# Performance work log

Measured on AMD Instinct MI355X. Metric: run time of the kernel, lower is better.

Reference implementation:

```python
import jax, jax.numpy as jnp
import numpy as np

N = 50000
E = 1600000
IN_DIM = 128
H = 8
D = 16  # out_dim per head


def setup_inputs() -> dict:
    key = jax.random.key(0)
    ks = jax.random.split(key, 9)
    h = jax.random.normal(ks[0], (N, IN_DIM), dtype=jnp.float32)
    src = jax.random.randint(ks[1], (E,), 0, N, dtype=jnp.int32)
    dst = jax.random.randint(ks[2], (E,), 0, N, dtype=jnp.int32)
    s = 1.0 / np.sqrt(IN_DIM)
    WQ = jax.random.uniform(ks[3], (IN_DIM, H * D), jnp.float32, -s, s)
    WK = jax.random.uniform(ks[4], (IN_DIM, H * D), jnp.float32, -s, s)
    WV = jax.random.uniform(ks[5], (IN_DIM, H * D), jnp.float32, -s, s)
    bQ = jax.random.uniform(ks[6], (H * D,), jnp.float32, -s, s)
    bK = jax.random.uniform(ks[7], (H * D,), jnp.float32, -s, s)
    bV = jax.random.uniform(ks[8], (H * D,), jnp.float32, -s, s)
    return {"h": h, "src": src, "dst": dst, "WQ": WQ, "WK": WK, "WV": WV,
            "bQ": bQ, "bK": bK, "bV": bV}


def reference(h, src, dst, WQ, WK, WV, bQ, bK, bV):
    # Node projections -> [N, H, D]
    Q = (h @ WQ + bQ).reshape(-1, H, D)
    K = (h @ WK + bK).reshape(-1, H, D)
    V = (h @ WV + bV).reshape(-1, H, D)
    # Edge scores: dot(K[src], Q[dst]) per head, scaled+clamped exp -> [E, H]
    scale = jnp.float32(np.sqrt(D))
    score = jnp.exp(jnp.clip(jnp.sum(K[src] * Q[dst], axis=-1) / scale, -5.0, 5.0))
    # Scatter-sum to destination nodes
    wV = jax.ops.segment_sum(score[:, :, None] * V[src], dst, num_segments=N)  # [N, H, D]
    z = jax.ops.segment_sum(score, dst, num_segments=N)  # [N, H]
    return wV / z[:, :, None]
```

## Files before the change

kernel.cpp:

```cpp
#include <hip/hip_runtime.h>

#define N_NODES 50000
#define N_PAD   50048
#define N_EDGES 1600000
#define HD 128
#define CHUNK 4096
#define NCHUNK ((N_EDGES + CHUNK - 1) / CHUNK)
#define NBUCKET ((N_NODES + 127) / 128)
#define PROJ_BLOCKS (N_PAD / 64)

typedef __attribute__((ext_vector_type(8))) short short8;
typedef __attribute__((ext_vector_type(4))) float floatx4;
typedef __attribute__((ext_vector_type(2))) float float2v;

union U4S8 { uint4 u; short8 s; };

__device__ __forceinline__ unsigned short f2bf(float f) {
    unsigned u = __float_as_uint(f);
    unsigned r = (u + 0x7fffu + ((u >> 16) & 1u)) >> 16;
    return (unsigned short)r;
}

__global__ __launch_bounds__(256) void k_chunkhist(
    const int* __restrict__ dst, int* __restrict__ chunkhist, int* __restrict__ btot,
    const float* __restrict__ WQ, const float* __restrict__ WK, const float* __restrict__ WV,
    unsigned short* __restrict__ Wf) {
    int t = threadIdx.x, c = blockIdx.x;
    if (c >= NCHUNK) {
        int tid = (c - NCHUNK) * 256 + t;
        int lane = tid & 63;
        int kstep = (tid >> 6) & 3;
        int ntile = tid >> 8;
        int g = ntile >> 3;
        int col = (ntile & 7) * 16 + (lane & 15);
        int k0 = kstep * 32 + (lane >> 4) * 8;
        const float* W = (g == 0) ? WQ : (g == 1) ? WK : WV;
        unsigned short r[8];
#pragma unroll
        for (int j = 0; j < 8; ++j)
            r[j] = f2bf(W[(size_t)(k0 + j) * HD + col]);
        *(uint4*)(Wf + (size_t)tid * 8) = *(uint4*)r;
        return;
    }
    __shared__ int hist[NBUCKET];
    for (int i = t; i < NBUCKET; i += 256) hist[i] = 0;
    __syncthreads();
    int e0 = c * CHUNK;
    int cnt = min(CHUNK, N_EDGES - e0);
    const uint4* d4 = (const uint4*)(dst + e0);
    int cnt4 = cnt >> 2;
    for (int i = t; i < cnt4; i += 256) {
        uint4 v = d4[i];
        atomicAdd(&hist[v.x >> 7], 1);
        atomicAdd(&hist[v.y >> 7], 1);
        atomicAdd(&hist[v.z >> 7], 1);
        atomicAdd(&hist[v.w >> 7], 1);
    }
    __syncthreads();
    for (int i = t; i < NBUCKET; i += 256) {
        int v = hist[i];
        chunkhist[c * NBUCKET + i] = v;
        if (v) atomicAdd(&btot[i], v);
    }
}

__global__ __launch_bounds__(256) void k_choff(const int* __restrict__ chunkhist,
                                               const int* __restrict__ btot,
                                               int* __restrict__ bucket_ptr,
                                               int* __restrict__ chunkoff) {
    int b = blockIdx.x, t = threadIdx.x;
    int x = 0;
    for (int i = t; i < NBUCKET; i += 256)
        if (i < b) x += btot[i];
    __shared__ int red[256];
    red[t] = x;
    __syncthreads();
    for (int off = 128; off > 0; off >>= 1) {
        if (t < off) red[t] += red[t + off];
        __syncthreads();
    }
    int base = red[0];
    if (t == 0) {
        bucket_ptr[b] = base;
        if (b == NBUCKET - 1) bucket_ptr[NBUCKET] = base + btot[b];
    }
    const int PER = (NCHUNK + 255) / 256;
    int c0 = t * PER;
    int v[PER];
    int s = 0;
#pragma unroll
    for (int i = 0; i < PER; ++i) {
        int c = c0 + i;
        v[i] = (c < NCHUNK) ? chunkhist[c * NBUCKET + b] : 0;
        s += v[i];
    }
    __shared__ int part[256];
    part[t] = s;
    __syncthreads();
    for (int off = 1; off < 256; off <<= 1) {
        int y = (t >= off) ? part[t - off] : 0;
        __syncthreads();
        part[t] += y;
        __syncthreads();
    }
    int run = base + part[t] - s;
#pragma unroll
    for (int i = 0; i < PER; ++i) {
        int c = c0 + i;
        if (c < NCHUNK) { chunkoff[c * NBUCKET + b] = run; run += v[i]; }
    }
}

__global__ __launch_bounds__(256) void k_scatter_proj(
    const int* __restrict__ src, const int* __restrict__ dst,
    const int* __restrict__ chunkoff, int* __restrict__ packed,
    const float* __restrict__ h, const unsigned short* __restrict__ Wf,
    const float* __restrict__ bQ, const float* __restrict__ bK, const float* __restrict__ bV,
    float* __restrict__ Qo, unsigned short* __restrict__ Kb, unsigned short* __restrict__ Vb) {
    int c = blockIdx.x;
    int t = threadIdx.x;
    if (c >= NCHUNK) {
        int blk = c - NCHUNK;
        int w = t >> 6;
        int l = t & 63;
        int row0 = blk * 64 + w * 16;
        int arow = row0 + (l & 15);
        int akoff = (l >> 4) * 8;
        bool rowok = arow < N_NODES;

        short8 a[4];
#pragma unroll
        for (int ks = 0; ks < 4; ++ks) {
            unsigned short r[8];
            if (rowok) {
                const float4* ap = (const float4*)(h + (size_t)arow * HD + ks * 32 + akoff);
                float4 f0 = ap[0], f1 = ap[1];
                r[0] = f2bf(f0.x); r[1] = f2bf(f0.y); r[2] = f2bf(f0.z); r[3] = f2bf(f0.w);
                r[4] = f2bf(f1.x); r[5] = f2bf(f1.y); r[6] = f2bf(f1.z); r[7] = f2bf(f1.w);
            } else {
#pragma unroll
                for (int j = 0; j < 8; ++j) r[j] = 0;
            }
            a[ks] = *(short8*)r;
        }

        int orow0 = row0 + (l >> 4) * 4;
#pragma unroll
        for (int nt = 0; nt < 24; ++nt) {
            floatx4 acc = (floatx4){0.f, 0.f, 0.f, 0.f};
#pragma unroll
            for (int ks = 0; ks < 4; ++ks) {
                U4S8 u;
                u.u = *(const uint4*)(Wf + ((size_t)(nt * 4 + ks) * 64 + l) * 8);
                acc = __builtin_amdgcn_mfma_f32_16x16x32_bf16(a[ks], u.s, acc, 0, 0, 0);
            }
            int g = nt >> 3;
            int cc = (nt & 7) * 16 + (l & 15);
            float bias = (g == 0) ? bQ[cc] : (g == 1) ? bK[cc] : bV[cc];
#pragma unroll
            for (int r = 0; r < 4; ++r) {
                int grow = orow0 + r;
                if (grow < N_NODES) {
                    float val = acc[r] + bias;
                    if (g == 0)      Qo[(size_t)grow * HD + cc] = val;
                    else if (g == 1) Kb[(size_t)grow * HD + cc] = f2bf(val);
                    else             Vb[(size_t)grow * HD + cc] = f2bf(val);
                }
            }
        }
        return;
    }
    __shared__ int cur[NBUCKET];
    for (int i = t; i < NBUCKET; i += 256) cur[i] = chunkoff[c * NBUCKET + i];
    __syncthreads();
    int e0 = c * CHUNK;
    int cnt = min(CHUNK, N_EDGES - e0);
    const uint4* d4 = (const uint4*)(dst + e0);
    const uint4* s4 = (const uint4*)(src + e0);
    int cnt4 = cnt >> 2;
    for (int i = t; i < cnt4; i += 256) {
        uint4 d = d4[i];
        uint4 s = s4[i];
        int pos;
        pos = atomicAdd(&cur[d.x >> 7], 1); packed[pos] = (s.x << 7) | (d.x & 127);
        pos = atomicAdd(&cur[d.y >> 7], 1); packed[pos] = (s.y << 7) | (d.y & 127);
        pos = atomicAdd(&cur[d.z >> 7], 1); packed[pos] = (s.z << 7) | (d.z & 127);
        pos = atomicAdd(&cur[d.w >> 7], 1); packed[pos] = (s.w << 7) | (d.w & 127);
    }
}

__global__ __launch_bounds__(256) void k_finalize(const int* __restrict__ bucket_ptr,
                                                  const int* __restrict__ packed,
                                                  int* __restrict__ row_ptr,
                                                  int* __restrict__ col_src) {
    __shared__ int hist[128], part[128], cur[128];
    int b = blockIdx.x, t = threadIdx.x;
    if (t < 128) hist[t] = 0;
    __syncthreads();
    int ebeg = bucket_ptr[b], eend = bucket_ptr[b + 1];
    int m = eend - ebeg;
    for (int i = t; i < m; i += 256)
        atomicAdd(&hist[packed[ebeg + i] & 127], 1);
    __syncthreads();
    int v = 0;
    if (t < 128) { v = hist[t]; part[t] = v; }
    __syncthreads();
    for (int off = 1; off < 128; off <<= 1) {
        int x = 0;
        if (t < 128 && t >= off) x = part[t - off];
        __syncthreads();
        if (t < 128) part[t] += x;
        __syncthreads();
    }
    if (t < 128) {
        int excl = part[t] - v;
        int node = b * 128 + t;
        if (node < N_NODES) row_ptr[node] = ebeg + excl;
        if (node == N_NODES - 1) row_ptr[N_NODES] = eend;
        cur[t] = ebeg + excl;
    }
    __syncthreads();
    for (int i = t; i < m; i += 256) {
        int p = packed[ebeg + i];
        int pos = atomicAdd(&cur[p & 127], 1);
        col_src[pos] = p >> 7;
    }
}


__device__ __forceinline__ float2v bf2f2(unsigned u) {
    float2v r;
    r.x = __uint_as_float(u << 16);
    r.y = __uint_as_float(u & 0xffff0000u);
    return r;
}
#define FMA2(a, b, c) __builtin_elementwise_fma((a), (b), (c))

#define LOADKV(K0, K1, V0, V1, blk)                                        \
    {                                                                      \
        int _s = __shfl(e_l, 8 * (blk) + o);                               \
        const uint4* _Kp = (const uint4*)(Kbp + (size_t)_s * HD);          \
        const uint4* _Vp = (const uint4*)(Vbp + (size_t)_s * HD);          \
        K0 = _Kp[0]; K1 = _Kp[1]; V0 = _Vp[0]; V1 = _Vp[1];                \
    }

#define STEPC(K0, K1, V0, V1, blk)                                         \
    {                                                                      \
        float2v d2 = FMA2(bf2f2(K0.x), qp0, Z2);                           \
        d2 = FMA2(bf2f2(K0.y), qp1, d2);                                   \
        d2 = FMA2(bf2f2(K0.z), qp2, d2);                                   \
        d2 = FMA2(bf2f2(K0.w), qp3, d2);                                   \
        d2 = FMA2(bf2f2(K1.x), qp4, d2);                                   \
        d2 = FMA2(bf2f2(K1.y), qp5, d2);                                   \
        d2 = FMA2(bf2f2(K1.z), qp6, d2);                                   \
        d2 = FMA2(bf2f2(K1.w), qp7, d2);                                   \
        float dot = d2.x + d2.y;                                           \
        float sc = __expf(fminf(fmaxf(dot * 0.25f, -5.f), 5.f));           \
        if (8 * (blk) + o >= mm) sc = 0.f;                                 \
        float2v sc2;                                                       \
        sc2.x = sc; sc2.y = sc;                                            \
        ac0 = FMA2(sc2, bf2f2(V0.x), ac0);                                 \
        ac1 = FMA2(sc2, bf2f2(V0.y), ac1);                                 \
        ac2 = FMA2(sc2, bf2f2(V0.z), ac2);                                 \
        ac3 = FMA2(sc2, bf2f2(V0.w), ac3);                                 \
        ac4 = FMA2(sc2, bf2f2(V1.x), ac4);                                 \
        ac5 = FMA2(sc2, bf2f2(V1.y), ac5);                                 \
        ac6 = FMA2(sc2, bf2f2(V1.z), ac6);                                 \
        ac7 = FMA2(sc2, bf2f2(V1.w), ac7);                                 \
        z += sc;                                                           \
    }

__global__ __launch_bounds__(256) void attn_kernel(
    const float* __restrict__ Q,
    const unsigned short* __restrict__ Kb, const unsigned short* __restrict__ Vb,
    const int* __restrict__ row_ptr, const int* __restrict__ col_src,
    float* __restrict__ out) {
    int n = blockIdx.x * 4 + (threadIdx.x >> 6);
    if (n >= N_NODES) return;
    int l = threadIdx.x & 63;
    int o = l >> 3;
    int p = l & 7;

    const unsigned short* Kbp = Kb + p * 16;
    const unsigned short* Vbp = Vb + p * 16;

    float2v Z2;
    Z2.x = 0.f; Z2.y = 0.f;

    const float4* Qv = (const float4*)(Q + (size_t)n * HD + p * 16);
    float4 q0 = Qv[0], q1 = Qv[1], q2 = Qv[2], q3 = Qv[3];
    float2v qp0, qp1, qp2, qp3, qp4, qp5, qp6, qp7;
    qp0.x = q0.x; qp0.y = q0.y;  qp1.x = q0.z; qp1.y = q0.w;
    qp2.x = q1.x; qp2.y = q1.y;  qp3.x = q1.z; qp3.y = q1.w;
    qp4.x = q2.x; qp4.y = q2.y;  qp5.x = q2.z; qp5.y = q2.w;
    qp6.x = q3.x; qp6.y = q3.y;  qp7.x = q3.z; qp7.y = q3.w;

    float2v ac0 = Z2, ac1 = Z2, ac2 = Z2, ac3 = Z2;
    float2v ac4 = Z2, ac5 = Z2, ac6 = Z2, ac7 = Z2;
    float z = 0.f;

    int beg = row_ptr[n], end = row_ptr[n + 1];

    for (int base = beg; base < end; base += 64) {
        int mm = min(64, end - base);
        int e_l = col_src[(base + l < end) ? (base + l) : beg];
        int steps = (mm + 7) >> 3;

        uint4 kA0, kA1, vA0, vA1;
        uint4 kB0, kB1, vB0, vB1;

        LOADKV(kA0, kA1, vA0, vA1, 0);
        int i = 0;
        while (true) {
            bool has1 = (i + 1 < steps);
            if (has1) LOADKV(kB0, kB1, vB0, vB1, i + 1);
            STEPC(kA0, kA1, vA0, vA1, i);
            if (!has1) break;
            if (i + 2 < steps) LOADKV(kA0, kA1, vA0, vA1, i + 2);
            STEPC(kB0, kB1, vB0, vB1, i + 1);
            i += 2;
            if (i >= steps) break;
        }
    }

#pragma unroll
    for (int j = 0; j < 8; ++j) {
        float2v* a = (j == 0) ? &ac0 : (j == 1) ? &ac1 : (j == 2) ? &ac2 :
                     (j == 3) ? &ac3 : (j == 4) ? &ac4 : (j == 5) ? &ac5 :
                     (j == 6) ? &ac6 : &ac7;
        a->x += __shfl_xor(a->x, 8);
        a->x += __shfl_xor(a->x, 16);
        a->x += __shfl_xor(a->x, 32);
        a->y += __shfl_xor(a->y, 8);
        a->y += __shfl_xor(a->y, 16);
        a->y += __shfl_xor(a->y, 32);
    }
    z += __shfl_xor(z, 8);
    z += __shfl_xor(z, 16);
    z += __shfl_xor(z, 32);

    if (o == 0) {
        float inv = 1.f / z;
        float4* O = (float4*)(out + (size_t)n * HD + p * 16);
        O[0] = (float4){ac0.x * inv, ac0.y * inv, ac1.x * inv, ac1.y * inv};
        O[1] = (float4){ac2.x * inv, ac2.y * inv, ac3.x * inv, ac3.y * inv};
        O[2] = (float4){ac4.x * inv, ac4.y * inv, ac5.x * inv, ac5.y * inv};
        O[3] = (float4){ac6.x * inv, ac6.y * inv, ac7.x * inv, ac7.y * inv};
    }
}


static inline char* align256(char* p) {
    return (char*)(((uintptr_t)p + 255) & ~(uintptr_t)255);
}

extern "C" void kernel_launch(void* const* d_in, const int* in_sizes, int n_in,
                              void* d_out, int out_size, void* d_ws, size_t ws_size,
                              hipStream_t stream) {
    const float* h  = (const float*)d_in[0];
    const int*   src = (const int*)d_in[1];
    const int*   dst = (const int*)d_in[2];
    const float* WQ = (const float*)d_in[3];
    const float* WK = (const float*)d_in[4];
    const float* WV = (const float*)d_in[5];
    const float* bQ = (const float*)d_in[6];
    const float* bK = (const float*)d_in[7];
    const float* bV = (const float*)d_in[8];
    float* out = (float*)d_out;

    char* p = (char*)d_ws;
    float* Q = (float*)p;                    p += (size_t)N_PAD * HD * 4;
    unsigned short* Kb = (unsigned short*)p; p += (size_t)N_PAD * HD * 2;
    unsigned short* Vb = (unsigned short*)p; p += (size_t)N_PAD * HD * 2;
    unsigned short* Wf = (unsigned short*)p; p += (size_t)24 * 4 * 64 * 8 * 2;
    p = align256(p);
    int* row_ptr    = (int*)p;               p += (N_NODES + 2) * 4;
    p = align256(p);
    int* bucket_ptr = (int*)p;               p += (NBUCKET + 1) * 4;
    p = align256(p);
    int* btot       = (int*)p;               p += NBUCKET * 4;
    p = align256(p);
    int* chunkhist  = (int*)p;               p += (size_t)NCHUNK * NBUCKET * 4;
    p = align256(p);
    int* chunkoff   = (int*)p;               p += (size_t)NCHUNK * NBUCKET * 4;
    p = align256(p);
    int* packed     = (int*)p;               p += (size_t)N_EDGES * 4;
    p = align256(p);
    int* col_src    = (int*)p;               p += (size_t)N_EDGES * 4;

    (void)hipMemsetAsync(btot, 0, NBUCKET * sizeof(int), stream);
    k_chunkhist<<<NCHUNK + 24, 256, 0, stream>>>(dst, chunkhist, btot, WQ, WK, WV, Wf);
    k_choff<<<NBUCKET, 256, 0, stream>>>(chunkhist, btot, bucket_ptr, chunkoff);
    k_scatter_proj<<<NCHUNK + PROJ_BLOCKS, 256, 0, stream>>>(
        src, dst, chunkoff, packed, h, Wf, bQ, bK, bV, Q, Kb, Vb);
    k_finalize<<<NBUCKET, 256, 0, stream>>>(bucket_ptr, packed, row_ptr, col_src);
    attn_kernel<<<(N_NODES + 3) / 4, 256, 0, stream>>>(Q, Kb, Vb, row_ptr, col_src, out);
}
```

Baseline: 271.8 us.

## Interleave K and V per head and deepen gather prefetch to three stages

K and V bf16 projections are now stored interleaved per head in one [N,256] buffer, so each lane's K and V slice for a source node sits in one contiguous 64-byte run instead of two separate 32-byte rows. The attention loop moves from double to triple buffering of the gathered K/V registers, issuing loads three steps ahead and clamping out-of-range prefetches to the last valid step. This aims to cut gather transactions and hide more memory latency, at the cost of more live registers, which may lower occupancy, and some redundant tail loads.

```diff
diff --git a/kernel.cpp b/kernel.cpp
--- a/kernel.cpp
+++ b/kernel.cpp
@@ -116,7 +116,7 @@
     const int* __restrict__ chunkoff, int* __restrict__ packed,
     const float* __restrict__ h, const unsigned short* __restrict__ Wf,
     const float* __restrict__ bQ, const float* __restrict__ bK, const float* __restrict__ bV,
-    float* __restrict__ Qo, unsigned short* __restrict__ Kb, unsigned short* __restrict__ Vb) {
+    float* __restrict__ Qo, unsigned short* __restrict__ KV) {
     int c = blockIdx.x;
     int t = threadIdx.x;
     if (c >= NCHUNK) {
@@ -157,14 +157,15 @@
             int g = nt >> 3;
             int cc = (nt & 7) * 16 + (l & 15);
             float bias = (g == 0) ? bQ[cc] : (g == 1) ? bK[cc] : bV[cc];
+            int headoff = (cc >> 4) * 32 + (cc & 15);
 #pragma unroll
             for (int r = 0; r < 4; ++r) {
                 int grow = orow0 + r;
                 if (grow < N_NODES) {
                     float val = acc[r] + bias;
                     if (g == 0)      Qo[(size_t)grow * HD + cc] = val;
-                    else if (g == 1) Kb[(size_t)grow * HD + cc] = f2bf(val);
-                    else             Vb[(size_t)grow * HD + cc] = f2bf(val);
+                    else if (g == 1) KV[(size_t)grow * 256 + headoff] = f2bf(val);
+                    else             KV[(size_t)grow * 256 + headoff + 16] = f2bf(val);
                 }
             }
         }
@@ -238,10 +239,10 @@
 
 #define LOADKV(K0, K1, V0, V1, blk)                                        \
     {                                                                      \
-        int _s = __shfl(e_l, 8 * (blk) + o);                               \
-        const uint4* _Kp = (const uint4*)(Kbp + (size_t)_s * HD);          \
-        const uint4* _Vp = (const uint4*)(Vbp + (size_t)_s * HD);          \
-        K0 = _Kp[0]; K1 = _Kp[1]; V0 = _Vp[0]; V1 = _Vp[1];                \
+        int _b = (blk) < smax ? (blk) : smax;                              \
+        int _s = __shfl(e_l, 8 * _b + o);                                  \
+        const uint4* _kv = (const uint4*)(KVp + (size_t)_s * 256);         \
+        K0 = _kv[0]; K1 = _kv[1]; V0 = _kv[2]; V1 = _kv[3];                \
     }
 
 #define STEPC(K0, K1, V0, V1, blk)                                         \
@@ -272,7 +273,7 @@
 
 __global__ __launch_bounds__(256) void attn_kernel(
     const float* __restrict__ Q,
-    const unsigned short* __restrict__ Kb, const unsigned short* __restrict__ Vb,
+    const unsigned short* __restrict__ KV,
     const int* __restrict__ row_ptr, const int* __restrict__ col_src,
     float* __restrict__ out) {
     int n = blockIdx.x * 4 + (threadIdx.x >> 6);
@@ -281,8 +282,7 @@
     int o = l >> 3;
     int p = l & 7;
 
-    const unsigned short* Kbp = Kb + p * 16;
-    const unsigned short* Vbp = Vb + p * 16;
+    const unsigned short* KVp = KV + p * 32;
 
     float2v Z2;
     Z2.x = 0.f; Z2.y = 0.f;
@@ -305,20 +305,27 @@
         int mm = min(64, end - base);
         int e_l = col_src[(base + l < end) ? (base + l) : beg];
         int steps = (mm + 7) >> 3;
-
-        uint4 kA0, kA1, vA0, vA1;
-        uint4 kB0, kB1, vB0, vB1;
-
-        LOADKV(kA0, kA1, vA0, vA1, 0);
+        int smax = steps - 1;
+
+        uint4 xK0, xK1, xV0, xV1;
+        uint4 yK0, yK1, yV0, yV1;
+        uint4 zK0, zK1, zV0, zV1;
+
+        LOADKV(xK0, xK1, xV0, xV1, 0);
+        LOADKV(yK0, yK1, yV0, yV1, 1);
+        LOADKV(zK0, zK1, zV0, zV1, 2);
+
         int i = 0;
         while (true) {
-            bool has1 = (i + 1 < steps);
-            if (has1) LOADKV(kB0, kB1, vB0, vB1, i + 1);
-            STEPC(kA0, kA1, vA0, vA1, i);
-            if (!has1) break;
-            if (i + 2 < steps) LOADKV(kA0, kA1, vA0, vA1, i + 2);
-            STEPC(kB0, kB1, vB0, vB1, i + 1);
-            i += 2;
+            STEPC(xK0, xK1, xV0, xV1, i);
+            LOADKV(xK0, xK1, xV0, xV1, i + 3);
+            if (i + 1 >= steps) break;
+            STEPC(yK0, yK1, yV0, yV1, i + 1);
+            LOADKV(yK0, yK1, yV0, yV1, i + 4);
+            if (i + 2 >= steps) break;
+            STEPC(zK0, zK1, zV0, zV1, i + 2);
+            LOADKV(zK0, zK1, zV0, zV1, i + 5);
+            i += 3;
             if (i >= steps) break;
         }
     }
@@ -370,8 +377,7 @@
 
     char* p = (char*)d_ws;
     float* Q = (float*)p;                    p += (size_t)N_PAD * HD * 4;
-    unsigned short* Kb = (unsigned short*)p; p += (size_t)N_PAD * HD * 2;
-    unsigned short* Vb = (unsigned short*)p; p += (size_t)N_PAD * HD * 2;
+    unsigned short* KV = (unsigned short*)p; p += (size_t)N_PAD * 256 * 2;
     unsigned short* Wf = (unsigned short*)p; p += (size_t)24 * 4 * 64 * 8 * 2;
     p = align256(p);
     int* row_ptr    = (int*)p;               p += (N_NODES + 2) * 4;
@@ -392,7 +398,7 @@
     k_chunkhist<<<NCHUNK + 24, 256, 0, stream>>>(dst, chunkhist, btot, WQ, WK, WV, Wf);
     k_choff<<<NBUCKET, 256, 0, stream>>>(chunkhist, btot, bucket_ptr, chunkoff);
     k_scatter_proj<<<NCHUNK + PROJ_BLOCKS, 256, 0, stream>>>(
-        src, dst, chunkoff, packed, h, Wf, bQ, bK, bV, Q, Kb, Vb);
+        src, dst, chunkoff, packed, h, Wf, bQ, bK, bV, Q, KV);
     k_finalize<<<NBUCKET, 256, 0, stream>>>(bucket_ptr, packed, row_ptr, col_src);
-    attn_kernel<<<(N_NODES + 3) / 4, 256, 0, stream>>>(Q, Kb, Vb, row_ptr, col_src, out);
-}
+    attn_kernel<<<(N_NODES + 3) / 4, 256, 0, stream>>>(Q, KV, row_ptr, col_src, out);
+}
```

Result: no change. 271.2 us (-0.2%).
